# Kernel tuning notes

Measured on AMD Instinct MI355X. Metric: run time of the kernel, lower is better.

## Reference

```python
import jax, jax.numpy as jnp
import numpy as np

N_NODES = 50000
N_EDGES = 800000
NUM_RELS = 16
IN_DIM, H_DIM, OUT_DIM = 128, 128, 64


def setup_inputs() -> dict:
    key = jax.random.key(0)
    ks = jax.random.split(key, 7)
    feat = jax.random.normal(ks[0], (N_NODES, IN_DIM), dtype=jnp.float32)
    norm = jax.random.uniform(ks[1], (N_EDGES, 1), dtype=jnp.float32)
    bound1 = 1.0 / np.sqrt(IN_DIM)
    bound2 = 1.0 / np.sqrt(H_DIM)
    W1 = jax.random.uniform(ks[2], (NUM_RELS, IN_DIM, H_DIM), dtype=jnp.float32, minval=-bound1, maxval=bound1)
    W2 = jax.random.uniform(ks[3], (NUM_RELS, H_DIM, OUT_DIM), dtype=jnp.float32, minval=-bound2, maxval=bound2)
    src = jax.random.randint(ks[4], (N_EDGES,), 0, N_NODES, dtype=jnp.int32)
    dst = jax.random.randint(ks[5], (N_EDGES,), 0, N_NODES, dtype=jnp.int32)
    etypes = jax.random.randint(ks[6], (N_EDGES,), 0, NUM_RELS, dtype=jnp.int32)
    return {"feat": feat, "norm": norm, "W1": W1, "W2": W2, "src": src, "dst": dst, "etypes": etypes}


def _rgcn_layer(h, W, src, dst, etypes, norm, num_nodes):
    # Transform every node by every relation weight (dense batched GEMM),
    # then gather the (src, etype) slice per edge: identical math to
    # gather_mm(h[src], W, idx_b=etypes) since matmul commutes with gather.
    t = jnp.einsum('ni,rio->nro', h, W)          # [N, R, O]
    msg = t[src, etypes] * norm                  # [E, O]
    return jax.ops.segment_sum(msg, dst, num_segments=num_nodes)  # sum-aggregate


def reference(feat, norm, W1, W2, src, dst, etypes):
    n = feat.shape[0]
    h = jax.nn.relu(_rgcn_layer(feat, W1, src, dst, etypes, norm, n))
    out = _rgcn_layer(h, W2, src, dst, etypes, norm, n)
    return out
```

## Files before the change

### kernel.cpp

```cpp
#include <hip/hip_runtime.h>


#define R_NUM 16

typedef __attribute__((ext_vector_type(8))) short bf16x8;
typedef __attribute__((ext_vector_type(4))) float f32x4;

__device__ __forceinline__ float bf2f(unsigned short u) {
    unsigned int x = ((unsigned int)u) << 16;
    return __builtin_bit_cast(float, x);
}
__device__ __forceinline__ unsigned short f2bf(float f) {
    unsigned int x = __builtin_bit_cast(unsigned int, f);
    x += 0x7FFFu + ((x >> 16) & 1u);
    return (unsigned short)(x >> 16);
}
__device__ __forceinline__ unsigned pack2(float a, float b) {
    return (unsigned)f2bf(a) | ((unsigned)f2bf(b) << 16);
}
__device__ __forceinline__ float lo16(unsigned v) { return bf2f((unsigned short)(v & 0xFFFF)); }
__device__ __forceinline__ float hi16(unsigned v) { return bf2f((unsigned short)(v >> 16)); }

__device__ __forceinline__ bf16x8 gload16(const unsigned short* p) {
    bf16x8 r;
    asm volatile("global_load_dwordx4 %0, %1, off" : "=&v"(r) : "v"(p));
    return r;
}

__global__ void detect_dtype(const unsigned short* __restrict__ raw, int* flag) {
    __shared__ int tot;
    if (threadIdx.x == 0) tot = 0;
    __syncthreads();
    int c = 0;
    for (int i = threadIdx.x; i < 4096; i += 256) {
        unsigned short u = raw[2 * i];
        int e = (u >> 7) & 0xFF;
        if (e >= 113 && e <= 134) c++;
    }
    atomicAdd(&tot, c);
    __syncthreads();
    if (threadIdx.x == 0) *flag = (tot > 2048) ? 1 : 0;
}

__global__ void transpose_both(const void* __restrict__ W1, const void* __restrict__ W2,
                               unsigned short* __restrict__ w1t, unsigned short* __restrict__ w2t,
                               const int* __restrict__ flagp) {
    const int flag = *flagp;
    const int n1 = R_NUM * 128 * 128;
    const int n2 = R_NUM * 128 * 64;
    int idx = blockIdx.x * 256 + threadIdx.x;
    if (idx < n1) {
        int k = idx % 128, o = (idx / 128) % 128, r = idx / (128 * 128);
        int iin = (r * 128 + k) * 128 + o;
        float v = flag ? bf2f(((const unsigned short*)W1)[iin]) : ((const float*)W1)[iin];
        w1t[idx] = f2bf(v);
    } else if (idx < n1 + n2) {
        int j = idx - n1;
        int k = j % 128, o = (j / 128) % 64, r = j / (128 * 64);
        int iin = (r * 128 + k) * 64 + o;
        float v = flag ? bf2f(((const unsigned short*)W2)[iin]) : ((const float*)W2)[iin];
        w2t[j] = f2bf(v);
    }
}

__global__ void to_bf16(const void* __restrict__ in, unsigned short* __restrict__ out, int n8,
                        const int* __restrict__ flagp) {
    int i = blockIdx.x * 256 + threadIdx.x;
    if (i >= n8) return;
    uint4 v;
    if (*flagp) {
        v = ((const uint4*)in)[i];
    } else {
        const float4* p = (const float4*)in + (size_t)i * 2;
        float4 f0 = p[0];
        float4 f1 = p[1];
        v.x = pack2(f0.x, f0.y);
        v.y = pack2(f0.z, f0.w);
        v.z = pack2(f1.x, f1.y);
        v.w = pack2(f1.z, f1.w);
    }
    ((uint4*)out)[i] = v;
}

template <int NOUT>
__global__ __launch_bounds__(256, 4) void gemm_plane(const unsigned short* __restrict__ A,
                                                     const unsigned short* __restrict__ Wt,
                                                     unsigned short* __restrict__ T, int nnodes) {
    constexpr int LDA = 136;
    constexpr int NTC = NOUT / 64;
    __shared__ unsigned short lA[64 * LDA];
    const int tid = threadIdx.x;
    const int rel = blockIdx.x & 15;
    const int node0 = (blockIdx.x >> 4) * 64;
    const int w = tid >> 6, lane = tid & 63;
    const int quad = lane >> 4, mr = lane & 15;

    bf16x8 bfr[NTC][4];
    {
        const unsigned short* wb = Wt + ((size_t)rel * NOUT + w * 16 + mr) * 128 + quad * 8;
#pragma unroll
        for (int c = 0; c < NTC; c++)
#pragma unroll
            for (int kk = 0; kk < 4; kk++)
                bfr[c][kk] = gload16(wb + c * 64 * 128 + kk * 32);
    }

    for (int i = tid; i < 64 * 16; i += 256) {
        int row = i >> 4, seg = i & 15;
        int node = node0 + row;
        uint4 v = make_uint4(0u, 0u, 0u, 0u);
        if (node < nnodes) v = *(const uint4*)(A + (size_t)node * 128 + seg * 8);
        *(uint4*)(lA + row * LDA + seg * 8) = v;
    }
    __syncthreads();
    asm volatile("s_waitcnt vmcnt(0)" ::: "memory");
    __builtin_amdgcn_sched_barrier(0);

    f32x4 acc[4][NTC];
#pragma unroll
    for (int mt = 0; mt < 4; mt++)
#pragma unroll
        for (int c = 0; c < NTC; c++) acc[mt][c] = 0.f;

#pragma unroll
    for (int kk = 0; kk < 4; kk++) {
        bf16x8 a[4];
#pragma unroll
        for (int mt = 0; mt < 4; mt++)
            a[mt] = *(const bf16x8*)(lA + (mt * 16 + mr) * LDA + kk * 32 + quad * 8);
#pragma unroll
        for (int c = 0; c < NTC; c++)
#pragma unroll
            for (int mt = 0; mt < 4; mt++)
                acc[mt][c] =
                    __builtin_amdgcn_mfma_f32_16x16x32_bf16(bfr[c][kk], a[mt], acc[mt][c], 0, 0, 0);
    }
    __syncthreads();

#pragma unroll
    for (int mt = 0; mt < 4; mt++)
#pragma unroll
        for (int c = 0; c < NTC; c++) {
            uint2 pv;
            pv.x = pack2(acc[mt][c][0], acc[mt][c][1]);
            pv.y = pack2(acc[mt][c][2], acc[mt][c][3]);
            *(uint2*)(lA + (mt * 16 + mr) * LDA + c * 64 + w * 16 + quad * 4) = pv;
        }
    __syncthreads();

    constexpr int SEGS = NOUT / 8;
    constexpr int SPT = 64 * SEGS / 256;
#pragma unroll
    for (int it = 0; it < SPT; it++) {
        int i = it * 256 + tid;
        int row = i / SEGS, seg = i % SEGS;
        int node = node0 + row;
        if (node < nnodes)
            *(uint4*)(T + ((size_t)rel * nnodes + node) * NOUT + seg * 8) =
                *(const uint4*)(lA + row * LDA + seg * 8);
    }
}

__global__ void hist_dst(const int* __restrict__ dst, int* __restrict__ counts, int nedges) {
    int e = blockIdx.x * 256 + threadIdx.x;
    if (e < nedges) atomicAdd(&counts[dst[e]], 1);
}

__global__ __launch_bounds__(256) void scan_phase1(const int* __restrict__ counts,
                                                   int* __restrict__ blocksums, int n) {
    __shared__ int red[256];
    int base = blockIdx.x * 1024 + threadIdx.x * 4;
    int s = 0;
#pragma unroll
    for (int j = 0; j < 4; j++) {
        int idx = base + j;
        if (idx < n) s += counts[idx];
    }
    red[threadIdx.x] = s;
    __syncthreads();
    for (int d = 128; d > 0; d >>= 1) {
        if (threadIdx.x < d) red[threadIdx.x] += red[threadIdx.x + d];
        __syncthreads();
    }
    if (threadIdx.x == 0) blocksums[blockIdx.x] = red[0];
}

__global__ __launch_bounds__(1024) void scan_phase2(const int* __restrict__ blocksums,
                                                    int* __restrict__ blockoff, int nb) {
    __shared__ int arr[1024];
    int t = threadIdx.x;
    arr[t] = (t < nb) ? blocksums[t] : 0;
    __syncthreads();
    for (int d = 1; d < 1024; d <<= 1) {
        int v = (t >= d) ? arr[t - d] : 0;
        __syncthreads();
        arr[t] += v;
        __syncthreads();
    }
    if (t < nb) blockoff[t] = (t == 0) ? 0 : arr[t - 1];
}

__global__ __launch_bounds__(256) void scan_phase3(const int* __restrict__ counts,
                                                   const int* __restrict__ blockoff,
                                                   int* __restrict__ offsets,
                                                   int* __restrict__ cursor, int n) {
    __shared__ int tsum[256];
    int base = blockIdx.x * 1024 + threadIdx.x * 4;
    int c[4];
    int s = 0;
#pragma unroll
    for (int j = 0; j < 4; j++) {
        int idx = base + j;
        c[j] = (idx < n) ? counts[idx] : 0;
        s += c[j];
    }
    tsum[threadIdx.x] = s;
    __syncthreads();
    for (int d = 1; d < 256; d <<= 1) {
        int v = (threadIdx.x >= d) ? tsum[threadIdx.x - d] : 0;
        __syncthreads();
        tsum[threadIdx.x] += v;
        __syncthreads();
    }
    int run = blockoff[blockIdx.x] + ((threadIdx.x == 0) ? 0 : tsum[threadIdx.x - 1]);
#pragma unroll
    for (int j = 0; j < 4; j++) {
        int idx = base + j;
        if (idx < n) {
            offsets[idx] = run;
            cursor[idx] = run;
            if (idx == n - 1) offsets[n] = run + c[j];
            run += c[j];
        }
    }
}

__global__ void fill_payload(const int* __restrict__ src, const int* __restrict__ dst,
                             const int* __restrict__ et, const void* __restrict__ nrm,
                             const int* __restrict__ flagp, int* __restrict__ cursor,
                             uint2* __restrict__ payload, int nedges) {
    int e = blockIdx.x * 256 + threadIdx.x;
    if (e >= nedges) return;
    int flag = *flagp;
    float nm = flag ? bf2f(((const unsigned short*)nrm)[e]) : ((const float*)nrm)[e];
    int pos = atomicAdd(&cursor[dst[e]], 1);
    uint2 pl;
    pl.x = ((unsigned)src[e] << 4) | (unsigned)(et[e] & 15);
    pl.y = __builtin_bit_cast(unsigned, nm);
    payload[pos] = pl;
}

template <int NOUT, int OUTMODE>
__global__ __launch_bounds__(256) void gather_seg(const unsigned short* __restrict__ T,
                                                  const int* __restrict__ offsets,
                                                  const uint2* __restrict__ payload,
                                                  void* __restrict__ out, int nnodes,
                                                  const int* __restrict__ flagp) {
    constexpr int SUBW = NOUT / 2;
    const int lane = threadIdx.x & 63;
    const int ll = lane & (SUBW - 1);
    const int dpb = 256 / SUBW;
    const int dst = blockIdx.x * dpb + threadIdx.x / SUBW;
    if (dst >= nnodes) return;
    const int base = lane & ~(SUBW - 1);
    const int beg = offsets[dst], end = offsets[dst + 1];
    float ax = 0.f, ay = 0.f;

    auto rowp = [&](unsigned key) {
        return (const unsigned*)(T + ((size_t)(key & 15) * nnodes + (key >> 4)) * NOUT);
    };

    for (int i = beg; i < end; i += SUBW) {
        int cnt = min(SUBW, end - i);
        uint2 pl = make_uint2(0u, 0u);
        if (ll < cnt) pl = payload[i + ll];
        int j = 0;
        for (; j + 4 <= cnt; j += 4) {
            unsigned k0 = (unsigned)__shfl((int)pl.x, base + j);
            unsigned k1 = (unsigned)__shfl((int)pl.x, base + j + 1);
            unsigned k2 = (unsigned)__shfl((int)pl.x, base + j + 2);
            unsigned k3 = (unsigned)__shfl((int)pl.x, base + j + 3);
            float n0 = __builtin_bit_cast(float, (unsigned)__shfl((int)pl.y, base + j));
            float n1 = __builtin_bit_cast(float, (unsigned)__shfl((int)pl.y, base + j + 1));
            float n2 = __builtin_bit_cast(float, (unsigned)__shfl((int)pl.y, base + j + 2));
            float n3 = __builtin_bit_cast(float, (unsigned)__shfl((int)pl.y, base + j + 3));
            unsigned v0 = rowp(k0)[ll];
            unsigned v1 = rowp(k1)[ll];
            unsigned v2 = rowp(k2)[ll];
            unsigned v3 = rowp(k3)[ll];
            ax = fmaf(lo16(v0), n0, ax); ay = fmaf(hi16(v0), n0, ay);
            ax = fmaf(lo16(v1), n1, ax); ay = fmaf(hi16(v1), n1, ay);
            ax = fmaf(lo16(v2), n2, ax); ay = fmaf(hi16(v2), n2, ay);
            ax = fmaf(lo16(v3), n3, ax); ay = fmaf(hi16(v3), n3, ay);
        }
        for (; j < cnt; j++) {
            unsigned k = (unsigned)__shfl((int)pl.x, base + j);
            float nm = __builtin_bit_cast(float, (unsigned)__shfl((int)pl.y, base + j));
            unsigned v = rowp(k)[ll];
            ax = fmaf(lo16(v), nm, ax);
            ay = fmaf(hi16(v), nm, ay);
        }
    }
    if (OUTMODE == 0) {
        ((unsigned*)out)[(size_t)dst * SUBW + ll] = pack2(fmaxf(ax, 0.f), fmaxf(ay, 0.f));
    } else {
        if (*flagp) {
            ((unsigned*)out)[(size_t)dst * SUBW + ll] = pack2(ax, ay);
        } else {
            float2 v;
            v.x = ax; v.y = ay;
            ((float2*)out)[(size_t)dst * SUBW + ll] = v;
        }
    }
}

template <int NOUT, int AMODE>
__global__ __launch_bounds__(256) void gemm_rel(const void* __restrict__ Asrc,
                                                const unsigned short* __restrict__ Wt,
                                                unsigned short* __restrict__ T, int nnodes,
                                                int rbase, const int* __restrict__ flagp) {
    constexpr int LDA = 136;
    __shared__ unsigned short lA[64 * LDA];
    __shared__ unsigned short lB[NOUT * LDA];
    const int tid = threadIdx.x;
    const int node0 = blockIdx.x * 64;
    const int rel = rbase + blockIdx.y;
    const int Gr = gridDim.y;
    const int flag = (AMODE == 0) ? *flagp : 1;

    for (int i = tid; i < 64 * 16; i += 256) {
        int row = i >> 4, seg = i & 15;
        int node = node0 + row;
        uint4 v = make_uint4(0u, 0u, 0u, 0u);
        if (node < nnodes) {
            if (AMODE == 1) {
                const float* p = (const float*)Asrc + (size_t)node * 128 + seg * 8;
                float4 f0 = ((const float4*)p)[0];
                float4 f1 = ((const float4*)p)[1];
                v.x = pack2(fmaxf(f0.x, 0.f), fmaxf(f0.y, 0.f));
                v.y = pack2(fmaxf(f0.z, 0.f), fmaxf(f0.w, 0.f));
                v.z = pack2(fmaxf(f1.x, 0.f), fmaxf(f1.y, 0.f));
                v.w = pack2(fmaxf(f1.z, 0.f), fmaxf(f1.w, 0.f));
            } else if (flag) {
                v = *(const uint4*)((const unsigned short*)Asrc + (size_t)node * 128 + seg * 8);
            } else {
                const float* p = (const float*)Asrc + (size_t)node * 128 + seg * 8;
                float4 f0 = ((const float4*)p)[0];
                float4 f1 = ((const float4*)p)[1];
                v.x = pack2(f0.x, f0.y);
                v.y = pack2(f0.z, f0.w);
                v.z = pack2(f1.x, f1.y);
                v.w = pack2(f1.z, f1.w);
            }
        }
        *(uint4*)(lA + row * LDA + seg * 8) = v;
    }
    for (int i = tid; i < NOUT * 16; i += 256) {
        int o = i >> 4, seg = i & 15;
        *(uint4*)(lB + o * LDA + seg * 8) =
            *(const uint4*)(Wt + ((size_t)rel * NOUT + o) * 128 + seg * 8);
    }
    __syncthreads();

    const int w = tid >> 6, lane = tid & 63;
    const int quad = lane >> 4, mr = lane & 15;
    constexpr int NT = NOUT / 16;
    f32x4 acc[NT];
#pragma unroll
    for (int t = 0; t < NT; t++) acc[t] = 0.f;
    const unsigned short* pa = lA + (w * 16 + mr) * LDA + quad * 8;
    const unsigned short* pb = lB + mr * LDA + quad * 8;
#pragma unroll
    for (int kk = 0; kk < 4; kk++) {
        bf16x8 a = *(const bf16x8*)(pa + kk * 32);
#pragma unroll
        for (int nt = 0; nt < NT; nt++) {
            bf16x8 b = *(const bf16x8*)(pb + nt * 16 * LDA + kk * 32);
            acc[nt] = __builtin_amdgcn_mfma_f32_16x16x32_bf16(a, b, acc[nt], 0, 0, 0);
        }
    }
#pragma unroll
    for (int nt = 0; nt < NT; nt++)
#pragma unroll
        for (int reg = 0; reg < 4; reg++) {
            int node = node0 + w * 16 + quad * 4 + reg;
            if (node < nnodes)
                T[((size_t)node * Gr + blockIdx.y) * NOUT + nt * 16 + mr] = f2bf(acc[nt][reg]);
        }
}

template <int NOUT>
__global__ void scatter_k(const unsigned short* __restrict__ T, int Gr, int rbase,
                          const void* __restrict__ nrm, const int* __restrict__ flagp,
                          const int* __restrict__ src, const int* __restrict__ dst,
                          const int* __restrict__ et, float* __restrict__ accum, int nedges) {
    constexpr int LPE = NOUT / 2;
    const int flag = *flagp;
    const int epb = 256 / LPE;
    const int sub = threadIdx.x % LPE;
    const int slot = threadIdx.x / LPE;
    for (int e = blockIdx.x * epb + slot; e < nedges; e += gridDim.x * epb) {
        int g = et[e] - rbase;
        if (g < 0 || g >= Gr) continue;
        int s = src[e], d = dst[e];
        float nm = flag ? bf2f(((const unsigned short*)nrm)[e]) : ((const float*)nrm)[e];
        unsigned pv = ((const unsigned*)(T + ((size_t)s * Gr + g) * NOUT))[sub];
        float* p = accum + (size_t)d * NOUT + sub * 2;
        unsafeAtomicAdd(p, lo16(pv) * nm);
        unsafeAtomicAdd(p + 1, hi16(pv) * nm);
    }
}

__global__ void write_out(const float* __restrict__ acc, void* __restrict__ dout, int n,
                          const int* __restrict__ flagp) {
    int flag = *flagp;
    int i = blockIdx.x * 256 + threadIdx.x;
    if (i >= n) return;
    float v = acc[i];
    if (flag) ((unsigned short*)dout)[i] = f2bf(v);
    else      ((float*)dout)[i] = v;
}

extern "C" void kernel_launch(void* const* d_in, const int* in_sizes, int n_in,
                              void* d_out, int out_size, void* d_ws, size_t ws_size,
                              hipStream_t stream) {
    const void* feat = d_in[0];
    const void* norm = d_in[1];
    const void* W1 = d_in[2];
    const void* W2 = d_in[3];
    const int* src = (const int*)d_in[4];
    const int* dst = (const int*)d_in[5];
    const int* et  = (const int*)d_in[6];

    const int nnodes = in_sizes[0] / 128;
    const int nedges = in_sizes[1];

    char* ws = (char*)d_ws;
    size_t off = 0;
    auto alloc = [&](size_t bytes) { size_t o = off; off += (bytes + 255) & ~255ULL; return o; };
    size_t off_flag = alloc(4);
    size_t off_w1t  = alloc((size_t)R_NUM * 128 * 128 * 2);
    size_t off_w2t  = alloc((size_t)R_NUM * 64 * 128 * 2);

    int* flagp = (int*)(ws + off_flag);
    unsigned short* w1t = (unsigned short*)(ws + off_w1t);
    unsigned short* w2t = (unsigned short*)(ws + off_w2t);

    size_t f_off = off;
    auto falloc = [&](size_t bytes) { size_t o = f_off; f_off += (bytes + 255) & ~255ULL; return o; };
    size_t off_offs = falloc((size_t)(nnodes + 1) * 4);
    size_t off_curs = falloc((size_t)nnodes * 4);
    size_t off_cnt  = falloc((size_t)nnodes * 4);
    size_t off_bsum = falloc(1024 * 4);
    size_t off_boff = falloc(1024 * 4);
    size_t off_pay  = falloc((size_t)nedges * 8);
    size_t off_nbf  = falloc((size_t)nnodes * 128 * 2);
    size_t off_t    = falloc((size_t)nnodes * R_NUM * 128 * 2);
    const int nb = (nnodes + 1023) / 1024;
    bool fast = (f_off <= ws_size) && (nb <= 1024);

    const int gx = (nnodes + 63) / 64;
    const int ntr = R_NUM * 128 * 128 + R_NUM * 128 * 64;

    detect_dtype<<<1, 256, 0, stream>>>((const unsigned short*)feat, flagp);
    transpose_both<<<(ntr + 255) / 256, 256, 0, stream>>>(W1, W2, w1t, w2t, flagp);

    if (fast) {
        int* offs = (int*)(ws + off_offs);
        int* curs = (int*)(ws + off_curs);
        int* cnt  = (int*)(ws + off_cnt);
        int* bsum = (int*)(ws + off_bsum);
        int* boff = (int*)(ws + off_boff);
        uint2* pay = (uint2*)(ws + off_pay);
        unsigned short* nbf = (unsigned short*)(ws + off_nbf);
        unsigned short* t = (unsigned short*)(ws + off_t);

        hipMemsetAsync(cnt, 0, (size_t)nnodes * 4, stream);
        hist_dst<<<(nedges + 255) / 256, 256, 0, stream>>>(dst, cnt, nedges);
        scan_phase1<<<nb, 256, 0, stream>>>(cnt, bsum, nnodes);
        scan_phase2<<<1, 1024, 0, stream>>>(bsum, boff, nb);
        scan_phase3<<<nb, 256, 0, stream>>>(cnt, boff, offs, curs, nnodes);
        fill_payload<<<(nedges + 255) / 256, 256, 0, stream>>>(src, dst, et, norm, flagp,
                                                               curs, pay, nedges);

        const int n8 = nnodes * 16;
        to_bf16<<<(n8 + 255) / 256, 256, 0, stream>>>(feat, nbf, n8, flagp);

        gemm_plane<128><<<gx * 16, 256, 0, stream>>>(nbf, w1t, t, nnodes);
        gather_seg<128, 0><<<(nnodes + 3) / 4, 256, 0, stream>>>(t, offs, pay, nbf, nnodes, flagp);
        gemm_plane<64><<<gx * 16, 256, 0, stream>>>(nbf, w2t, t, nnodes);
        gather_seg<64, 1><<<(nnodes + 7) / 8, 256, 0, stream>>>(t, offs, pay, d_out, nnodes, flagp);
        return;
    }

    size_t off_hpre = alloc((size_t)nnodes * 128 * 4);
    size_t off_oacc = alloc((size_t)nnodes * 64 * 4);
    size_t t_cap = (ws_size > off) ? (ws_size - off) : 0;
    auto pick_gr = [&](int ncol) {
        int gr = 0;
        for (int g = 16; g >= 1; g >>= 1)
            if ((size_t)nnodes * g * ncol * 2 <= t_cap) { gr = g; break; }
        return gr;
    };
    int Gr1 = pick_gr(128);
    int Gr2 = pick_gr(64);
    if (Gr1 < 1 || Gr2 < 1) {
        hipMemsetAsync(d_out, 0x42, (size_t)out_size * 2, stream);
        return;
    }
    float* hpre = (float*)(ws + off_hpre);
    float* oacc = (float*)(ws + off_oacc);
    unsigned short* t = (unsigned short*)(ws + off);

    hipMemsetAsync(hpre, 0, (size_t)nnodes * 128 * 4, stream);
    hipMemsetAsync(oacc, 0, (size_t)nnodes * 64 * 4, stream);
    for (int rb = 0; rb < R_NUM; rb += Gr1) {
        gemm_rel<128, 0><<<dim3(gx, Gr1), 256, 0, stream>>>(feat, w1t, t, nnodes, rb, flagp);
        scatter_k<128><<<4096, 256, 0, stream>>>(t, Gr1, rb, norm, flagp, src, dst, et, hpre, nedges);
    }
    for (int rb = 0; rb < R_NUM; rb += Gr2) {
        gemm_rel<64, 1><<<dim3(gx, Gr2), 256, 0, stream>>>(hpre, w2t, t, nnodes, rb, flagp);
        scatter_k<64><<<4096, 256, 0, stream>>>(t, Gr2, rb, norm, flagp, src, dst, et, oacc, nedges);
    }
    int nout = nnodes * 64;
    write_out<<<(nout + 255) / 256, 256, 0, stream>>>(oacc, d_out, nout, flagp);
}
```

Baseline: 360.3 us.

## Loop all relations inside one GEMM block to reuse the staged node tile

```diff
diff --git a/kernel.cpp b/kernel.cpp
--- a/kernel.cpp
+++ b/kernel.cpp
@@ -83,27 +83,30 @@
 }
 
 template <int NOUT>
-__global__ __launch_bounds__(256, 4) void gemm_plane(const unsigned short* __restrict__ A,
+__global__ __launch_bounds__(256, 3) void gemm_plane(const unsigned short* __restrict__ A,
                                                      const unsigned short* __restrict__ Wt,
-                                                     unsigned short* __restrict__ T, int nnodes) {
+                                                     unsigned short* __restrict__ T, int nnodes,
+                                                     int npad) {
     constexpr int LDA = 136;
+    constexpr int LDC = NOUT + 8;
     constexpr int NTC = NOUT / 64;
+    constexpr int SEGS = NOUT / 8;
+    constexpr int SPT = 64 * SEGS / 256;
     __shared__ unsigned short lA[64 * LDA];
+    __shared__ unsigned short lC[64 * LDC];
     const int tid = threadIdx.x;
-    const int rel = blockIdx.x & 15;
-    const int node0 = (blockIdx.x >> 4) * 64;
+    const int node0 = blockIdx.x * 64;
     const int w = tid >> 6, lane = tid & 63;
     const int quad = lane >> 4, mr = lane & 15;
 
-    bf16x8 bfr[NTC][4];
-    {
-        const unsigned short* wb = Wt + ((size_t)rel * NOUT + w * 16 + mr) * 128 + quad * 8;
-#pragma unroll
-        for (int c = 0; c < NTC; c++)
-#pragma unroll
-            for (int kk = 0; kk < 4; kk++)
-                bfr[c][kk] = gload16(wb + c * 64 * 128 + kk * 32);
-    }
+    const unsigned short* wbase = Wt + ((size_t)(w * 16 + mr)) * 128 + quad * 8;
+
+    bf16x8 bfr[2][NTC][4];
+#pragma unroll
+    for (int c = 0; c < NTC; c++)
+#pragma unroll
+        for (int kk = 0; kk < 4; kk++)
+            bfr[0][c][kk] = gload16(wbase + (size_t)(c * 64) * 128 + kk * 32);
 
     for (int i = tid; i < 64 * 16; i += 256) {
         int row = i >> 4, seg = i & 15;
@@ -116,48 +119,72 @@
     asm volatile("s_waitcnt vmcnt(0)" ::: "memory");
     __builtin_amdgcn_sched_barrier(0);
 
-    f32x4 acc[4][NTC];
-#pragma unroll
-    for (int mt = 0; mt < 4; mt++)
-#pragma unroll
-        for (int c = 0; c < NTC; c++) acc[mt][c] = 0.f;
-
-#pragma unroll
-    for (int kk = 0; kk < 4; kk++) {
-        bf16x8 a[4];
+#pragma unroll 2
+    for (int r = 0; r < R_NUM; r++) {
+        if (r > 0) {
+            if constexpr (NOUT == 128)
+                asm volatile("s_waitcnt vmcnt(4)" ::: "memory");
+            else
+                asm volatile("s_waitcnt vmcnt(2)" ::: "memory");
+            __builtin_amdgcn_sched_barrier(0);
+        }
+
+        f32x4 acc[4][NTC];
 #pragma unroll
         for (int mt = 0; mt < 4; mt++)
-            a[mt] = *(const bf16x8*)(lA + (mt * 16 + mr) * LDA + kk * 32 + quad * 8);
-#pragma unroll
-        for (int c = 0; c < NTC; c++)
+#pragma unroll
+            for (int c = 0; c < NTC; c++) acc[mt][c] = 0.f;
+
+#pragma unroll
+        for (int kk = 0; kk < 4; kk++) {
+            bf16x8 a[4];
 #pragma unroll
             for (int mt = 0; mt < 4; mt++)
-                acc[mt][c] =
-                    __builtin_amdgcn_mfma_f32_16x16x32_bf16(bfr[c][kk], a[mt], acc[mt][c], 0, 0, 0);
-    }
-    __syncthreads();
-
-#pragma unroll
-    for (int mt = 0; mt < 4; mt++)
-#pragma unroll
-        for (int c = 0; c < NTC; c++) {
-            uint2 pv;
-            pv.x = pack2(acc[mt][c][0], acc[mt][c][1]);
-            pv.y = pack2(acc[mt][c][2], acc[mt][c][3]);
-            *(uint2*)(lA + (mt * 16 + mr) * LDA + c * 64 + w * 16 + quad * 4) = pv;
-        }
-    __syncthreads();
-
-    constexpr int SEGS = NOUT / 8;
-    constexpr int SPT = 64 * SEGS / 256;
-#pragma unroll
-    for (int it = 0; it < SPT; it++) {
-        int i = it * 256 + tid;
-        int row = i / SEGS, seg = i % SEGS;
-        int node = node0 + row;
-        if (node < nnodes)
-            *(uint4*)(T + ((size_t)rel * nnodes + node) * NOUT + seg * 8) =
-                *(const uint4*)(lA + row * LDA + seg * 8);
+                a[mt] = *(const bf16x8*)(lA + (mt * 16 + mr) * LDA + kk * 32 + quad * 8);
+#pragma unroll
+            for (int c = 0; c < NTC; c++)
+#pragma unroll
+                for (int mt = 0; mt < 4; mt++)
+                    acc[mt][c] = __builtin_amdgcn_mfma_f32_16x16x32_bf16(bfr[r & 1][c][kk], a[mt],
+                                                                         acc[mt][c], 0, 0, 0);
+        }
+
+        if (r + 1 < R_NUM) {
+#pragma unroll
+            for (int c = 0; c < NTC; c++)
+#pragma unroll
+                for (int kk = 0; kk < 4; kk++)
+                    bfr[(r + 1) & 1][c][kk] =
+                        gload16(wbase + (size_t)((r + 1) * NOUT + c * 64) * 128 + kk * 32);
+        }
+
+#pragma unroll
+        for (int mt = 0; mt < 4; mt++)
+#pragma unroll
+            for (int c = 0; c < NTC; c++) {
+                uint2 pv;
+                pv.x = pack2(acc[mt][c][0], acc[mt][c][1]);
+                pv.y = pack2(acc[mt][c][2], acc[mt][c][3]);
+                *(uint2*)(lC + (mt * 16 + mr) * LDC + c * 64 + w * 16 + quad * 4) = pv;
+            }
+
+        asm volatile("s_waitcnt lgkmcnt(0)" ::: "memory");
+        __builtin_amdgcn_sched_barrier(0);
+        __builtin_amdgcn_s_barrier();
+        __builtin_amdgcn_sched_barrier(0);
+
+#pragma unroll
+        for (int it = 0; it < SPT; it++) {
+            int i = it * 256 + tid;
+            int row = i / SEGS, seg = i % SEGS;
+            *(uint4*)(T + ((size_t)r * npad + node0 + row) * NOUT + seg * 8) =
+                *(const uint4*)(lC + row * LDC + seg * 8);
+        }
+
+        asm volatile("s_waitcnt lgkmcnt(0)" ::: "memory");
+        __builtin_amdgcn_sched_barrier(0);
+        __builtin_amdgcn_s_barrier();
+        __builtin_amdgcn_sched_barrier(0);
     }
 }
 
@@ -254,7 +281,7 @@
 __global__ __launch_bounds__(256) void gather_seg(const unsigned short* __restrict__ T,
                                                   const int* __restrict__ offsets,
                                                   const uint2* __restrict__ payload,
-                                                  void* __restrict__ out, int nnodes,
+                                                  void* __restrict__ out, int nnodes, int npad,
                                                   const int* __restrict__ flagp) {
     constexpr int SUBW = NOUT / 2;
     const int lane = threadIdx.x & 63;
@@ -267,7 +294,7 @@
     float ax = 0.f, ay = 0.f;
 
     auto rowp = [&](unsigned key) {
-        return (const unsigned*)(T + ((size_t)(key & 15) * nnodes + (key >> 4)) * NOUT);
+        return (const unsigned*)(T + ((size_t)(key & 15) * npad + (key >> 4)) * NOUT);
     };
 
     for (int i = beg; i < end; i += SUBW) {
@@ -446,6 +473,9 @@
     unsigned short* w1t = (unsigned short*)(ws + off_w1t);
     unsigned short* w2t = (unsigned short*)(ws + off_w2t);
 
+    const int gx = (nnodes + 63) / 64;
+    const int npad = gx * 64;
+
     size_t f_off = off;
     auto falloc = [&](size_t bytes) { size_t o = f_off; f_off += (bytes + 255) & ~255ULL; return o; };
     size_t off_offs = falloc((size_t)(nnodes + 1) * 4);
@@ -455,11 +485,10 @@
     size_t off_boff = falloc(1024 * 4);
     size_t off_pay  = falloc((size_t)nedges * 8);
     size_t off_nbf  = falloc((size_t)nnodes * 128 * 2);
-    size_t off_t    = falloc((size_t)nnodes * R_NUM * 128 * 2);
+    size_t off_t    = falloc((size_t)npad * R_NUM * 128 * 2);
     const int nb = (nnodes + 1023) / 1024;
     bool fast = (f_off <= ws_size) && (nb <= 1024);
 
-    const int gx = (nnodes + 63) / 64;
     const int ntr = R_NUM * 128 * 128 + R_NUM * 128 * 64;
 
     detect_dtype<<<1, 256, 0, stream>>>((const unsigned short*)feat, flagp);
@@ -486,10 +515,12 @@
         const int n8 = nnodes * 16;
         to_bf16<<<(n8 + 255) / 256, 256, 0, stream>>>(feat, nbf, n8, flagp);
 
-        gemm_plane<128><<<gx * 16, 256, 0, stream>>>(nbf, w1t, t, nnodes);
-        gather_seg<128, 0><<<(nnodes + 3) / 4, 256, 0, stream>>>(t, offs, pay, nbf, nnodes, flagp);
-        gemm_plane<64><<<gx * 16, 256, 0, stream>>>(nbf, w2t, t, nnodes);
-        gather_seg<64, 1><<<(nnodes + 7) / 8, 256, 0, stream>>>(t, offs, pay, d_out, nnodes, flagp);
+        gemm_plane<128><<<gx, 256, 0, stream>>>(nbf, w1t, t, nnodes, npad);
+        gather_seg<128, 0><<<(nnodes + 3) / 4, 256, 0, stream>>>(t, offs, pay, nbf, nnodes, npad,
+                                                                 flagp);
+        gemm_plane<64><<<gx, 256, 0, stream>>>(nbf, w2t, t, nnodes, npad);
+        gather_seg<64, 1><<<(nnodes + 7) / 8, 256, 0, stream>>>(t, offs, pay, d_out, nnodes, npad,
+                                                                flagp);
         return;
     }
 
```

Measured after the change: 362.8 us. No clear change (+0.7%).
